# Performance work log

Hardware: AMD Instinct MI355X
Metric: run time of the kernel (lower is better)

The kernel has to match this reference:

```python
import jax, jax.numpy as jnp
import numpy as np

EPS = 1e-5  # RMSNorm epsilon


def rmsnorm(x, w):
    return x * jax.lax.rsqrt(jnp.mean(x * x, axis=-1, keepdims=True) + EPS) * w


def mamba_forward(u, in_proj_w, conv_w, conv_b, x_proj_w, dt_proj_w, dt_proj_b,
                  A_log, D_param, mamba_out_w):
    # u: (b, L, dm) -- canonical Mamba block (expand=2, d_state=16, d_conv=4)
    b, L, dm = u.shape
    di, ds = A_log.shape
    dtr = dt_proj_w.shape[1]
    xz = jnp.einsum('bld,ed->ble', u, in_proj_w)          # (b,L,2*di)
    x_, z = jnp.split(xz, 2, axis=-1)                     # each (b,L,di)
    # causal depthwise conv over the sequence axis
    dconv = conv_w.shape[-1]
    xc = jnp.transpose(x_, (0, 2, 1))                     # (b,di,L)
    xc = jnp.pad(xc, ((0, 0), (0, 0), (dconv - 1, 0)))
    xc = jax.lax.conv_general_dilated(xc, conv_w, window_strides=(1,), padding='VALID',
                                      dimension_numbers=('NCH', 'OIH', 'NCH'),
                                      feature_group_count=di)
    xc = xc + conv_b[None, :, None]
    x_ = jax.nn.silu(jnp.transpose(xc, (0, 2, 1)))        # (b,L,di)
    # input-dependent dt, B, C
    x_dbl = jnp.einsum('bld,ed->ble', x_, x_proj_w)       # (b,L,dtr+2*ds)
    dt, B, C = jnp.split(x_dbl, [dtr, dtr + ds], axis=-1)
    delta = jax.nn.softplus(jnp.einsum('blr,dr->bld', dt, dt_proj_w) + dt_proj_b)  # (b,L,di)
    A = -jnp.exp(A_log)                                   # (di,ds)

    def step(h, inp):
        d_t, B_t, C_t, x_t = inp                          # (b,di),(b,ds),(b,ds),(b,di)
        dA = jnp.exp(d_t[:, :, None] * A)                 # (b,di,ds)
        h = dA * h + (d_t * x_t)[:, :, None] * B_t[:, None, :]
        y = jnp.einsum('bds,bs->bd', h, C_t)
        return h, y

    xs = (jnp.moveaxis(delta, 1, 0), jnp.moveaxis(B, 1, 0),
          jnp.moveaxis(C, 1, 0), jnp.moveaxis(x_, 1, 0))
    h0 = jnp.zeros((b, di, ds), dtype=u.dtype)
    _, ys = jax.lax.scan(step, h0, xs)                    # ys: (L,b,di)
    y = jnp.moveaxis(ys, 0, 1) + x_ * D_param             # (b,L,di)
    y = y * jax.nn.silu(z)
    return jnp.einsum('bld,od->blo', y, mamba_out_w)      # (b,L,dm)


def conv1x1(W, bvec, t):
    # t: (b, cin, L) -> (b, cout, L)
    return jnp.einsum('oi,bit->bot', W, t) + bvec[None, :, None]


def reference(x, w_norm1, w_norm2, W_ip, b_ip, W_fp, b_fp, W_wp, b_wp, W_op, b_op,
              in_proj_w, conv_w, conv_b, x_proj_w, dt_proj_w, dt_proj_b,
              A_log, D_param, mamba_out_w):
    # x: (b, L, D) -- module's (b, c, l) with l == input_dim = D, c == seq = L
    residual = x
    xn = rmsnorm(x, w_norm1)                 # RMSNorm over last (input_dim) axis
    xt = jnp.transpose(xn, (0, 2, 1))        # 'b c l -> b l c' : (b, D, L)
    ssm = conv1x1(W_ip, b_ip, xt)            # (b, 2D, L)
    ssm = conv1x1(W_fp, b_fp, ssm)           # (b, 2D, L)
    u = jnp.transpose(ssm, (0, 2, 1))        # (b, L, 2D): seq=L, d_model=2D
    m = mamba_forward(u, in_proj_w, conv_w, conv_b, x_proj_w, dt_proj_w, dt_proj_b,
                      A_log, D_param, mamba_out_w)
    m = rmsnorm(m, w_norm2) + u              # PostNormMamba residual
    ssm = jnp.transpose(m, (0, 2, 1))        # (b, 2D, L)
    w = conv1x1(W_wp, b_wp, xt)              # (b, 2D, L)
    w = w * jax.nn.sigmoid(w)                # swish
    out = conv1x1(W_op, b_op, w * ssm)       # (b, D, L)
    return jnp.transpose(out, (0, 2, 1)) + residual


def setup_inputs():
    key = jax.random.key(0)
    ks = jax.random.split(key, 16)
    D, L, b = 64, 4096, 4
    dm, di, ds, dconv = 2 * D, 4 * D, 16, 4
    dtr = (dm + 15) // 16  # dt_rank = ceil(d_model/16) = 8

    def n(k, shape, fan_in):
        return jax.random.normal(k, shape, jnp.float32) * (1.0 / np.sqrt(fan_in))

    return {
        'x': jax.random.normal(ks[0], (b, L, D), jnp.float32),
        'w_norm1': jnp.ones((D,), jnp.float32),
        'w_norm2': jnp.ones((dm,), jnp.float32),
        'W_ip': n(ks[1], (2 * D, D), D), 'b_ip': jnp.zeros((2 * D,), jnp.float32),
        'W_fp': n(ks[2], (2 * D, 2 * D), 2 * D), 'b_fp': jnp.zeros((2 * D,), jnp.float32),
        'W_wp': n(ks[3], (2 * D, D), D), 'b_wp': jnp.zeros((2 * D,), jnp.float32),
        'W_op': n(ks[4], (D, 2 * D), 2 * D), 'b_op': jnp.zeros((D,), jnp.float32),
        'in_proj_w': n(ks[5], (2 * di, dm), dm),
        'conv_w': n(ks[6], (di, 1, dconv), dconv),
        'conv_b': jnp.zeros((di,), jnp.float32),
        'x_proj_w': n(ks[7], (dtr + 2 * ds, di), di),
        'dt_proj_w': n(ks[8], (di, dtr), dtr),
        'dt_proj_b': jnp.full((di,), float(np.log(np.expm1(0.01))), jnp.float32),
        'A_log': jnp.log(jnp.broadcast_to(jnp.arange(1, ds + 1, dtype=jnp.float32), (di, ds))),
        'D_param': jnp.ones((di,), jnp.float32),
        'mamba_out_w': n(ks[9], (dm, di), di),
    }
```

## Files before the change

kernel.cpp:

```cpp
#include <hip/hip_runtime.h>
#include <hip/hip_bf16.h>

typedef __hip_bfloat16 bf16;
typedef __attribute__((ext_vector_type(8))) short bf16x8;
typedef __attribute__((ext_vector_type(4))) float f32x4;
#define DEV __device__ __forceinline__

constexpr int SEQ  = 4096;
constexpr int NB   = 4;
constexpr int NTOK = NB * SEQ;
constexpr float EPS = 1e-5f;
constexpr int NCH = 32;
constexpr int NCHUNK = SEQ / NCH;
constexpr float LOG2E = 1.44269504f;

constexpr int OFF_WDT  = 0;
constexpr int OFF_WB   = 2048;
constexpr int WB_IP = 0;
constexpr int WB_WP = 8192;
constexpr int WB_FP = 16384;
constexpr int WB_PR = 32768;
constexpr int WB_MO = 98304;
constexpr int WB_OP = 131072;
constexpr int WB_XP = 139264;
constexpr int WB_TOT = 151552;
constexpr int OFF_XDBL = OFF_WB + WB_TOT / 2;
constexpr int OFF_R1   = OFF_XDBL + NTOK * 40;
constexpr int OFF_WSW  = OFF_R1   + 1048576;
constexpr int OFF_U    = OFF_WSW  + 1048576;
constexpr int OFF_R2   = OFF_U    + 1048576;
constexpr int OFF_SILUZ= OFF_R2   + 2097152;
constexpr int OFF_XC   = OFF_SILUZ+ 2097152;
constexpr int OFF_G    = OFF_XC   + 2097152;
constexpr int OFF_FLAG = OFF_G    + 2097152;
constexpr int OFF_SUMM = OFF_FLAG + 16;
constexpr int OFF_HIN  = OFF_SUMM + 64 * NCHUNK * 256 * 2;
constexpr int OFF_PLOC = OFF_HIN  + 64 * NCHUNK * 256;
constexpr int OFF_CUMD = OFF_PLOC + NTOK * 256;

DEV float b2f(bf16 x) { return __bfloat162float(x); }
DEV bf16 f2b(float x) { return __float2bfloat16(x); }
DEV short shof(bf16 h) { short s; __builtin_memcpy(&s, &h, 2); return s; }
DEV float ldin(const void* p, int i, int f) {
  return f ? ((const float*)p)[i] : b2f(((const bf16*)p)[i]);
}
DEV unsigned pack2(float a, float b) {
  bf16 ha = f2b(a), hb = f2b(b);
  unsigned short ua, ub;
  __builtin_memcpy(&ua, &ha, 2); __builtin_memcpy(&ub, &hb, 2);
  return (unsigned)ua | ((unsigned)ub << 16);
}
DEV float lo16f(unsigned u) { return __int_as_float((int)(u << 16)); }
DEV float hi16f(unsigned u) { return __int_as_float((int)(u & 0xffff0000u)); }
template<int CTRL>
DEV float dpp_add(float v) {
  int r = __builtin_amdgcn_update_dpp(0, __float_as_int(v), CTRL, 0xF, 0xF, false);
  return v + __int_as_float(r);
}
DEV float exp2f_fast(float a) { return __builtin_amdgcn_exp2f(a); }
DEV float softplus(float a) {
  return (a > 20.f) ? a : __logf(1.f + exp2f_fast(a * LOG2E));
}
DEV float silu(float a) { return a / (1.f + __expf(-a)); }

DEV void cpw(int e, int base, int count, const void* __restrict__ src,
             bf16* __restrict__ wb, int f) {
  int r = e - base;
  if (r >= 0 && r < count) wb[base + r] = f2b(ldin(src, r, f));
}
__global__ __launch_bounds__(256) void prep_k(
    const void* __restrict__ w_ip, const void* __restrict__ w_wp, const void* __restrict__ w_fp,
    const void* __restrict__ w_pr, const void* __restrict__ w_mo, const void* __restrict__ w_op,
    const void* __restrict__ w_x,  const void* __restrict__ w_dt,
    const void* __restrict__ x, float* __restrict__ wsf, int* __restrict__ flagp)
{
  __shared__ int cnt;
  if (threadIdx.x == 0) cnt = 0;
  __syncthreads();
  {
    float v = b2f(((const bf16*)x)[threadIdx.x]);
    int ok = (v == v) && fabsf(v) > 1e-4f && fabsf(v) < 100.f;
    atomicAdd(&cnt, ok);
  }
  __syncthreads();
  int f = (cnt > 204) ? 0 : 1;
  if (blockIdx.x == 0 && threadIdx.x == 0) *flagp = f;

  int e = blockIdx.x * 256 + threadIdx.x;
  bf16* wb = (bf16*)(wsf + OFF_WB);
  cpw(e, WB_IP, 8192,  w_ip, wb, f);
  cpw(e, WB_WP, 8192,  w_wp, wb, f);
  cpw(e, WB_FP, 16384, w_fp, wb, f);
  cpw(e, WB_PR, 65536, w_pr, wb, f);
  cpw(e, WB_MO, 32768, w_mo, wb, f);
  cpw(e, WB_OP, 8192,  w_op, wb, f);
  {
    int r = e - WB_XP;
    if (r >= 0 && r < 12288) wb[WB_XP + r] = (r < 10240) ? f2b(ldin(w_x, r, f)) : f2b(0.f);
  }
  if (e < 2048) {
    int r = e >> 8, d = e & 255;
    wsf[OFF_WDT + e] = ldin(w_dt, d * 8 + r, f);
  }
}

__global__ __launch_bounds__(512) void fm_k(
    const void* __restrict__ x, const void* __restrict__ w1, const float* __restrict__ wsf,
    const void* __restrict__ b_ip, const void* __restrict__ b_wp, const void* __restrict__ b_fp,
    bf16* __restrict__ wsw, bf16* __restrict__ u, bf16* __restrict__ xpre,
    bf16* __restrict__ siluz, const int* __restrict__ flagp)
{
  __shared__ __align__(16) char smem[33280];
  short* xn   = (short*)smem;
  short* t1   = (short*)(smem + 4608);
  short* ul   = (short*)(smem + 13312);
  short* wswl = (short*)(smem + 22016);
  short* xzl  = (short*)smem;

  const int f = *flagp;
  const int tid = threadIdx.x;
  const int tok0 = blockIdx.x * 32;
  {
    const int token = tid >> 4, r = tid & 15;
    float v[4]; float ss = 0.f;
    #pragma unroll
    for (int k = 0; k < 4; ++k) {
      v[k] = ldin(x, (tok0 + token) * 64 + r * 4 + k, f);
      ss += v[k] * v[k];
    }
    ss += __shfl_xor(ss, 1, 16); ss += __shfl_xor(ss, 2, 16);
    ss += __shfl_xor(ss, 4, 16); ss += __shfl_xor(ss, 8, 16);
    float sc = rsqrtf(ss * (1.f / 64.f) + EPS);
    unsigned* dst = (unsigned*)xn + token * 36 + r * 2;
    #pragma unroll
    for (int k = 0; k < 2; ++k) {
      int i = r * 4 + k * 2;
      dst[k] = pack2(v[k*2] * sc * ldin(w1, i, f), v[k*2+1] * sc * ldin(w1, i + 1, f));
    }
  }
  __syncthreads();
  const int lane = tid & 63, m = lane & 15, q = lane >> 4;
  const int w = tid >> 6;
  {
    const int wt = w >> 2, ng = w & 3;
    const bf16* W = (const bf16*)(wsf + OFF_WB) + (wt ? WB_WP : WB_IP);
    const void* bia = wt ? b_wp : b_ip;
    bf16x8 a[2][2];
    #pragma unroll
    for (int mt = 0; mt < 2; ++mt)
      #pragma unroll
      for (int kk = 0; kk < 2; ++kk)
        a[mt][kk] = *(const bf16x8*)&xn[(mt * 16 + m) * 72 + kk * 32 + q * 8];
    #pragma unroll
    for (int nti = 0; nti < 2; ++nti) {
      int nt = ng * 2 + nti;
      int n = nt * 16 + m;
      f32x4 acc[2] = {{0,0,0,0},{0,0,0,0}};
      #pragma unroll
      for (int kk = 0; kk < 2; ++kk) {
        bf16x8 b = *(const bf16x8*)(W + (nt * 16 + m) * 64 + kk * 32 + q * 8);
        #pragma unroll
        for (int mt = 0; mt < 2; ++mt)
          acc[mt] = __builtin_amdgcn_mfma_f32_16x16x32_bf16(a[mt][kk], b, acc[mt], 0, 0, 0);
      }
      float bv = ldin(bia, n, f);
      #pragma unroll
      for (int mt = 0; mt < 2; ++mt)
        #pragma unroll
        for (int r = 0; r < 4; ++r) {
          float v = acc[mt][r] + bv;
          int row = mt * 16 + q * 4 + r;
          if (wt) wswl[row * 128 + n] = shof(f2b(silu(v)));
          else    t1[row * 136 + n] = shof(f2b(v));
        }
    }
  }
  __syncthreads();
  {
    int row = tid >> 4, c8 = (tid & 15) * 8;
    uint4 v = *(const uint4*)&wswl[row * 128 + c8];
    *(uint4*)(wsw + (tok0 + row) * 128 + c8) = v;
  }
  {
    const bf16* WF = (const bf16*)(wsf + OFF_WB) + WB_FP;
    bf16x8 a[2][4];
    #pragma unroll
    for (int mt = 0; mt < 2; ++mt)
      #pragma unroll
      for (int kk = 0; kk < 4; ++kk)
        a[mt][kk] = *(const bf16x8*)&t1[(mt * 16 + m) * 136 + kk * 32 + q * 8];
    {
      int nt = w;
      int n = nt * 16 + m;
      f32x4 acc[2] = {{0,0,0,0},{0,0,0,0}};
      #pragma unroll
      for (int kk = 0; kk < 4; ++kk) {
        bf16x8 b = *(const bf16x8*)(WF + (nt * 16 + m) * 128 + kk * 32 + q * 8);
        #pragma unroll
        for (int mt = 0; mt < 2; ++mt)
          acc[mt] = __builtin_amdgcn_mfma_f32_16x16x32_bf16(a[mt][kk], b, acc[mt], 0, 0, 0);
      }
      float bv = ldin(b_fp, n, f);
      #pragma unroll
      for (int mt = 0; mt < 2; ++mt)
        #pragma unroll
        for (int r = 0; r < 4; ++r)
          ul[(mt * 16 + q * 4 + r) * 136 + n] = shof(f2b(acc[mt][r] + bv));
    }
  }
  __syncthreads();
  {
    int row = tid >> 4, c8 = (tid & 15) * 8;
    uint4 v = *(const uint4*)&ul[row * 136 + c8];
    *(uint4*)(u + (tok0 + row) * 128 + c8) = v;
  }
  {
    const bf16* WP = (const bf16*)(wsf + OFF_WB) + WB_PR;
    bf16x8 a[2][4];
    #pragma unroll
    for (int mt = 0; mt < 2; ++mt)
      #pragma unroll
      for (int kk = 0; kk < 4; ++kk)
        a[mt][kk] = *(const bf16x8*)&ul[(mt * 16 + m) * 136 + kk * 32 + q * 8];
    __syncthreads();
    #pragma unroll
    for (int nti = 0; nti < 4; ++nti) {
      int nt = w * 4 + nti;
      int n = nt * 16 + m;
      f32x4 acc[2] = {{0,0,0,0},{0,0,0,0}};
      #pragma unroll
      for (int kk = 0; kk < 4; ++kk) {
        bf16x8 b = *(const bf16x8*)(WP + (nt * 16 + m) * 128 + kk * 32 + q * 8);
        #pragma unroll
        for (int mt = 0; mt < 2; ++mt)
          acc[mt] = __builtin_amdgcn_mfma_f32_16x16x32_bf16(a[mt][kk], b, acc[mt], 0, 0, 0);
      }
      #pragma unroll
      for (int mt = 0; mt < 2; ++mt)
        #pragma unroll
        for (int r = 0; r < 4; ++r) {
          int row = mt * 16 + q * 4 + r;
          float v = acc[mt][r];
          xzl[row * 520 + n] = shof(f2b(n < 256 ? v : silu(v)));
        }
    }
  }
  __syncthreads();
  {
    #pragma unroll
    for (int k = 0; k < 4; ++k) {
      int chunk = tid + k * 512;
      int row = chunk >> 6, seg = chunk & 63;
      uint4 v = *(const uint4*)&xzl[row * 520 + seg * 8];
      int n0 = seg * 8;
      if (n0 < 256) *(uint4*)(xpre + (tok0 + row) * 256 + n0) = v;
      else          *(uint4*)(siluz + (tok0 + row) * 256 + (n0 - 256)) = v;
    }
  }
}

__global__ __launch_bounds__(256) void conv_k(
    const bf16* __restrict__ xpre, const void* __restrict__ cw, const void* __restrict__ cb,
    const float* __restrict__ wsf, bf16* __restrict__ xc, float* __restrict__ xdbl,
    const int* __restrict__ flagp)
{
  __shared__ short xh[35 * 256];
  __shared__ short cs[32 * 264];
  const int f = *flagp;
  const int tid = threadIdx.x;
  const int tok0 = blockIdx.x * 32;
  const bool seqstart = (tok0 & (SEQ - 1)) == 0;
  for (int c = tid; c < 1120; c += 256) {
    int e0 = c * 8;
    int tt = e0 >> 8, i = e0 & 255;
    int gtok = tok0 + tt - 3;
    uint4* dst = (uint4*)(xh + e0);
    if (gtok >= 0 && !(seqstart && tt < 3)) *dst = *(const uint4*)(xpre + gtok * 256 + i);
    else                                    *dst = make_uint4(0, 0, 0, 0);
  }
  __syncthreads();
  {
    const int ch0 = (tid & 63) * 4;
    const int t0 = (tid >> 6) * 8;
    float w4[4][4], cb4[4];
    #pragma unroll
    for (int c = 0; c < 4; ++c) {
      cb4[c] = ldin(cb, ch0 + c, f);
      #pragma unroll
      for (int k = 0; k < 4; ++k) w4[c][k] = ldin(cw, (ch0 + c) * 4 + k, f);
    }
    float win[11][4];
    #pragma unroll
    for (int r = 0; r < 11; ++r) {
      uint2 v = *(const uint2*)&xh[(t0 + r) * 256 + ch0];
      win[r][0] = lo16f(v.x); win[r][1] = hi16f(v.x);
      win[r][2] = lo16f(v.y); win[r][3] = hi16f(v.y);
    }
    #pragma unroll
    for (int t = 0; t < 8; ++t) {
      unsigned pk[2];
      #pragma unroll
      for (int cp = 0; cp < 2; ++cp) {
        float o[2];
        #pragma unroll
        for (int ci = 0; ci < 2; ++ci) {
          int c = cp * 2 + ci;
          float acc = cb4[c];
          #pragma unroll
          for (int k = 0; k < 4; ++k) acc = fmaf(win[t + k][c], w4[c][k], acc);
          o[ci] = silu(acc);
        }
        pk[cp] = pack2(o[0], o[1]);
      }
      uint2 pv = make_uint2(pk[0], pk[1]);
      *(uint2*)&cs[(t0 + t) * 264 + ch0] = pv;
      *(uint2*)(xc + (tok0 + t0 + t) * 256 + ch0) = pv;
    }
  }
  __syncthreads();
  const int w = tid >> 6;
  if (w < 2) {
    const bf16* Wx = (const bf16*)(wsf + OFF_WB) + WB_XP;
    const int lane = tid & 63, m = lane & 15, quad = lane >> 4;
    f32x4 acc[3] = {{0,0,0,0},{0,0,0,0},{0,0,0,0}};
    #pragma unroll
    for (int k0 = 0; k0 < 256; k0 += 32) {
      bf16x8 af = *(const bf16x8*)&cs[(w * 16 + m) * 264 + k0 + quad * 8];
      #pragma unroll
      for (int nt = 0; nt < 3; ++nt) {
        bf16x8 bfr = *(const bf16x8*)(Wx + (nt * 16 + m) * 256 + k0 + quad * 8);
        acc[nt] = __builtin_amdgcn_mfma_f32_16x16x32_bf16(af, bfr, acc[nt], 0, 0, 0);
      }
    }
    #pragma unroll
    for (int nt = 0; nt < 3; ++nt) {
      int n = nt * 16 + m;
      if (n < 40) {
        #pragma unroll
        for (int r = 0; r < 4; ++r)
          xdbl[(tok0 + w * 16 + quad * 4 + r) * 40 + n] = acc[nt][r];
      }
    }
  }
}

__global__ __launch_bounds__(256) void scanF_k(
    const float* __restrict__ xdbl, const bf16* __restrict__ xc,
    const void* __restrict__ A_log, const void* __restrict__ dt_b,
    const float* __restrict__ WDT, float* __restrict__ summ,
    float* __restrict__ ploc, float* __restrict__ cumd, const int* __restrict__ flagp)
{
  const int f = *flagp;
  const int tid = threadIdx.x;
  const int bb = blockIdx.x >> 2, dgsup = blockIdx.x & 3, c = blockIdx.y;
  const int dgsub = tid >> 6, lane = tid & 63, dl = lane >> 2, squad = lane & 3;
  const int dg = dgsup * 4 + dgsub;
  const int bxOld = bb * 16 + dg;
  const int d_comp = dg * 16 + dl;
  const int bd = tid & 63;
  const int d_stg = dgsup * 64 + bd;
  const int bdc = dgsub * 16 + dl;
  const int tok_base = bb * SEQ + c * NCH;

  __shared__ float dt_l[NCH * 8];
  __shared__ float dx_l[16 * 64 * 2];
  __shared__ float Bp[16 * 16];
  __shared__ float Cp[16 * 16];
  __shared__ float pg_l[16 * 64];
  __shared__ float cd_l[16 * 64];

  float Aval2[4];
  #pragma unroll
  for (int j = 0; j < 4; ++j)
    Aval2[j] = -__expf(ldin(A_log, d_comp * 16 + squad * 4 + j, f)) * LOG2E;
  const float dtb_stg = ldin(dt_b, d_stg, f);
  float wdt[8];
  #pragma unroll
  for (int r = 0; r < 8; ++r) wdt[r] = WDT[r * 256 + d_stg];

  float h[4] = {0.f, 0.f, 0.f, 0.f};
  float sdlt = 0.f;

  if (tid < 64)
    *(float4*)(dt_l + tid * 4) = *(const float4*)(xdbl + (tok_base + (tid >> 1)) * 40 + (tid & 1) * 4);

  #pragma unroll 1
  for (int half = 0; half < 2; ++half) {
    const int tb = half * 16;
    __syncthreads();
    {
      int tl = tid >> 4, s = tid & 15;
      int tok = tok_base + tb + tl;
      Bp[tid] = xdbl[tok * 40 + 8 + s];
      Cp[tid] = xdbl[tok * 40 + 24 + s];
    }
    #pragma unroll
    for (int k = 0; k < 4; ++k) {
      int tl = (tid >> 6) + k * 4;
      int tok = tok_base + tb + tl;
      const float* dtr = dt_l + (tb + tl) * 8;
      float a = dtb_stg;
      #pragma unroll
      for (int r = 0; r < 8; ++r) a = fmaf(dtr[r], wdt[r], a);
      float dlt = softplus(a);
      float xcv = b2f(xc[tok * 256 + d_stg]);
      *(float2*)(dx_l + (tl * 64 + bd) * 2) = make_float2(dlt, dlt * xcv);
    }
    __syncthreads();

    #pragma unroll 8
    for (int tl = 0; tl < 16; ++tl) {
      float2 dx = *(const float2*)(dx_l + (tl * 64 + bdc) * 2);
      float4 B4 = *(const float4*)(Bp + tl * 16 + squad * 4);
      float Bv[4] = {B4.x, B4.y, B4.z, B4.w};
      #pragma unroll
      for (int j = 0; j < 4; ++j) {
        float dA = exp2f_fast(dx.x * Aval2[j]);
        h[j] = fmaf(dA, h[j], dx.y * Bv[j]);
      }
      sdlt += dx.x;
      float4 C4 = *(const float4*)(Cp + tl * 16 + squad * 4);
      float p = h[0] * C4.x;
      p = fmaf(h[1], C4.y, p);
      p = fmaf(h[2], C4.z, p);
      p = fmaf(h[3], C4.w, p);
      p = dpp_add<0xB1>(p);
      p = dpp_add<0x4E>(p);
      if (squad == 0) { pg_l[tl * 64 + bdc] = p; cd_l[tl * 64 + bdc] = sdlt; }
    }
    __syncthreads();
    #pragma unroll
    for (int k = 0; k < 4; ++k) {
      int tl = (tid >> 6) + k * 4;
      int tok = tok_base + tb + tl;
      ploc[tok * 256 + d_stg] = pg_l[tl * 64 + bd];
      cumd[tok * 256 + d_stg] = cd_l[tl * 64 + bd];
    }
  }

  float* dst = summ + ((bxOld * NCHUNK + c) * 256 + dl * 16 + squad * 4) * 2;
  *(float4*)(dst)     = make_float4(exp2f_fast(Aval2[0] * sdlt), h[0],
                                    exp2f_fast(Aval2[1] * sdlt), h[1]);
  *(float4*)(dst + 4) = make_float4(exp2f_fast(Aval2[2] * sdlt), h[2],
                                    exp2f_fast(Aval2[3] * sdlt), h[3]);
}

__global__ __launch_bounds__(256) void scanB_k(const float* __restrict__ summ, float* __restrict__ hinit) {
  int bx = blockIdx.x, qq = threadIdx.x;
  float h = 0.f;
  for (int c0 = 0; c0 < NCHUNK; c0 += 16) {
    float2 sv[16];
    #pragma unroll
    for (int k = 0; k < 16; ++k)
      sv[k] = *(const float2*)(summ + ((bx * NCHUNK + c0 + k) * 256 + qq) * 2);
    #pragma unroll
    for (int k = 0; k < 16; ++k) {
      hinit[(bx * NCHUNK + c0 + k) * 256 + qq] = h;
      h = fmaf(sv[k].x, h, sv[k].y);
    }
  }
}

__global__ __launch_bounds__(512) void backC_k(
    const float* __restrict__ xdbl, const bf16* __restrict__ xc, const bf16* __restrict__ siluz,
    const void* __restrict__ A_log, const void* __restrict__ D_par,
    const float* __restrict__ hinit, const float* __restrict__ ploc, const float* __restrict__ cumd,
    const float* __restrict__ wsf, const void* __restrict__ w2,
    const bf16* __restrict__ u, const bf16* __restrict__ wsw, const void* __restrict__ b_op,
    const void* __restrict__ x, void* __restrict__ out, const int* __restrict__ flagp)
{
  __shared__ __align__(16) char smem[51712];
  short* gl  = (short*)smem;
  float* Cp  = (float*)(smem + 16896);
  float* cdl = (float*)(smem + 18944);
  float* gcl = (float*)(smem + 35328);
  short* ms  = (short*)(smem + 18944);

  const int f = *flagp;
  const int tid = threadIdx.x;
  const int tok0 = blockIdx.x * 32;
  const int bb = tok0 >> 12;
  const int c  = (tok0 & (SEQ - 1)) >> 5;
  const int w = tid >> 6, lane = tid & 63;
  const int dl = lane >> 2, squad = lane & 3;
  const int chL = w * 16 + dl;
  const int chE = tid & 127;

  {
    int tl = tid >> 4, s = tid & 15;
    Cp[tid] = xdbl[(tok0 + tl) * 40 + 24 + s];
  }

  #pragma unroll 1
  for (int p = 0; p < 2; ++p) {
    const int ch = p * 128 + chL;
    #pragma unroll
    for (int k = 0; k < 8; ++k) {
      int tl = (tid >> 7) + k * 4;
      cdl[tl * 128 + chE] = cumd[(tok0 + tl) * 256 + p * 128 + chE];
    }
    float Aval2[4];
    #pragma unroll
    for (int j = 0; j < 4; ++j)
      Aval2[j] = -__expf(ldin(A_log, ch * 16 + squad * 4 + j, f)) * LOG2E;
    float4 hv = *(const float4*)(hinit +
        ((bb * 16 + (ch >> 4)) * NCHUNK + c) * 256 + (ch & 15) * 16 + squad * 4);
    __syncthreads();
    #pragma unroll 8
    for (int tl = 0; tl < 32; ++tl) {
      float cum = cdl[tl * 128 + chL];
      float4 C4 = *(const float4*)(Cp + tl * 16 + squad * 4);
      float pv =      C4.x * exp2f_fast(cum * Aval2[0]) * hv.x;
      pv = fmaf(C4.y * exp2f_fast(cum * Aval2[1]), hv.y, pv);
      pv = fmaf(C4.z * exp2f_fast(cum * Aval2[2]), hv.z, pv);
      pv = fmaf(C4.w * exp2f_fast(cum * Aval2[3]), hv.w, pv);
      pv = dpp_add<0xB1>(pv);
      pv = dpp_add<0x4E>(pv);
      if (squad == 0) gcl[tl * 128 + chL] = pv;
    }
    __syncthreads();
    {
      const int gch = p * 128 + chE;
      const float Dp = ldin(D_par, gch, f);
      #pragma unroll
      for (int k = 0; k < 8; ++k) {
        int tl = (tid >> 7) + k * 4;
        int tok = tok0 + tl;
        float pf = gcl[tl * 128 + chE] + ploc[tok * 256 + gch];
        float xcv = b2f(xc[tok * 256 + gch]);
        gl[tl * 264 + gch] = shof(f2b((pf + xcv * Dp) * b2f(siluz[tok * 256 + gch])));
      }
    }
    __syncthreads();
  }

  const int m = lane & 15, q = lane >> 4;
  const bf16* WM = (const bf16*)(wsf + OFF_WB) + WB_MO;
  const bf16* WO = (const bf16*)(wsf + OFF_WB) + WB_OP;
  {
    f32x4 acc[2] = {{0,0,0,0},{0,0,0,0}};
    #pragma unroll
    for (int kk = 0; kk < 8; ++kk) {
      bf16x8 a0 = *(const bf16x8*)&gl[m * 264 + kk * 32 + q * 8];
      bf16x8 a1 = *(const bf16x8*)&gl[(16 + m) * 264 + kk * 32 + q * 8];
      int nt = w;
      bf16x8 b = *(const bf16x8*)(WM + (nt * 16 + m) * 256 + kk * 32 + q * 8);
      acc[0] = __builtin_amdgcn_mfma_f32_16x16x32_bf16(a0, b, acc[0], 0, 0, 0);
      acc[1] = __builtin_amdgcn_mfma_f32_16x16x32_bf16(a1, b, acc[1], 0, 0, 0);
    }
    {
      int n = w * 16 + m;
      #pragma unroll
      for (int mt = 0; mt < 2; ++mt)
        #pragma unroll
        for (int r = 0; r < 4; ++r)
          ms[(mt * 16 + q * 4 + r) * 136 + n] = shof(f2b(acc[mt][r]));
    }
  }
  __syncthreads();
  {
    const int token = tid >> 4, r = tid & 15;
    float mv[8]; float ss = 0.f;
    #pragma unroll
    for (int k = 0; k < 8; ++k) {
      mv[k] = b2f(((const bf16*)ms)[token * 136 + r * 8 + k]);
      ss += mv[k] * mv[k];
    }
    ss += __shfl_xor(ss, 1, 16); ss += __shfl_xor(ss, 2, 16);
    ss += __shfl_xor(ss, 4, 16); ss += __shfl_xor(ss, 8, 16);
    float sc = rsqrtf(ss * (1.f / 128.f) + EPS);
    #pragma unroll
    for (int k = 0; k < 8; ++k) {
      int i = r * 8 + k;
      int ga = (tok0 + token) * 128 + i;
      float v = mv[k] * sc * ldin(w2, i, f) + b2f(u[ga]);
      ms[token * 136 + i] = shof(f2b(v * b2f(wsw[ga])));
    }
  }
  __syncthreads();
  {
    const int mt = w >> 2, nt = w & 3;
    bf16x8 a[4];
    #pragma unroll
    for (int kk = 0; kk < 4; ++kk)
      a[kk] = *(const bf16x8*)&ms[(mt * 16 + m) * 136 + kk * 32 + q * 8];
    __syncthreads();
    f32x4 acc = {0,0,0,0};
    #pragma unroll
    for (int kk = 0; kk < 4; ++kk) {
      bf16x8 b = *(const bf16x8*)(WO + (nt * 16 + m) * 128 + kk * 32 + q * 8);
      acc = __builtin_amdgcn_mfma_f32_16x16x32_bf16(a[kk], b, acc, 0, 0, 0);
    }
    float* outl = (float*)ms;
    int n = nt * 16 + m;
    #pragma unroll
    for (int r = 0; r < 4; ++r)
      outl[(mt * 16 + q * 4 + r) * 68 + n] = acc[r];
  }
  __syncthreads();
  {
    const float* outl = (const float*)ms;
    int row = tid >> 4, c0 = (tid & 15) * 4;
    float v[4];
    #pragma unroll
    for (int j = 0; j < 4; ++j)
      v[j] = outl[row * 68 + c0 + j] + ldin(b_op, c0 + j, f)
           + ldin(x, (tok0 + row) * 64 + c0 + j, f);
    if (f) {
      *(float4*)((float*)out + (tok0 + row) * 64 + c0) = make_float4(v[0], v[1], v[2], v[3]);
    } else {
      uint2 pv = make_uint2(pack2(v[0], v[1]), pack2(v[2], v[3]));
      *(uint2*)((bf16*)out + (tok0 + row) * 64 + c0) = pv;
    }
  }
}

extern "C" void kernel_launch(void* const* d_in, const int* in_sizes, int n_in,
                              void* d_out, int out_size, void* d_ws, size_t ws_size,
                              hipStream_t stream) {
  (void)in_sizes; (void)n_in; (void)out_size; (void)ws_size;
  const void* x        = d_in[0];
  const void* w_norm1  = d_in[1];
  const void* w_norm2  = d_in[2];
  const void* W_ip     = d_in[3];
  const void* b_ip     = d_in[4];
  const void* W_fp     = d_in[5];
  const void* b_fp     = d_in[6];
  const void* W_wp     = d_in[7];
  const void* b_wp     = d_in[8];
  const void* W_op     = d_in[9];
  const void* b_op     = d_in[10];
  const void* in_proj  = d_in[11];
  const void* conv_w   = d_in[12];
  const void* conv_b   = d_in[13];
  const void* x_proj   = d_in[14];
  const void* dt_projw = d_in[15];
  const void* dt_projb = d_in[16];
  const void* A_log    = d_in[17];
  const void* D_par    = d_in[18];
  const void* mo_w     = d_in[19];

  float* wsf    = (float*)d_ws;
  float* xdbl   = wsf + OFF_XDBL;
  bf16*  wsw_b  = (bf16*)(wsf + OFF_WSW);
  bf16*  u_b    = (bf16*)(wsf + OFF_U);
  bf16*  xpre_b = (bf16*)(wsf + OFF_R2);
  float* summ   = wsf + OFF_SUMM;
  float* hin    = wsf + OFF_HIN;
  float* plocp  = wsf + OFF_PLOC;
  float* cumdp  = wsf + OFF_CUMD;
  bf16*  siluz_b= (bf16*)(wsf + OFF_SILUZ);
  bf16*  xc_b   = (bf16*)(wsf + OFF_XC);
  int*   flagp  = (int*)(wsf + OFF_FLAG);

  prep_k<<<dim3(592), dim3(256), 0, stream>>>(W_ip, W_wp, W_fp, in_proj, mo_w, W_op,
                                              x_proj, dt_projw, x, wsf, flagp);
  fm_k<<<dim3(NTOK / 32), dim3(512), 0, stream>>>(x, w_norm1, wsf, b_ip, b_wp, b_fp,
                                                  wsw_b, u_b, xpre_b, siluz_b, flagp);
  conv_k<<<dim3(NTOK / 32), dim3(256), 0, stream>>>(xpre_b, conv_w, conv_b, wsf, xc_b, xdbl, flagp);
  scanF_k<<<dim3(16, NCHUNK), dim3(256), 0, stream>>>(xdbl, xc_b, A_log, dt_projb,
                                                      wsf + OFF_WDT, summ, plocp, cumdp, flagp);
  scanB_k<<<dim3(64), dim3(256), 0, stream>>>(summ, hin);
  backC_k<<<dim3(NTOK / 32), dim3(512), 0, stream>>>(xdbl, xc_b, siluz_b, A_log, D_par,
                                                     hin, plocp, cumdp, wsf, w_norm2,
                                                     u_b, wsw_b, b_op, x, d_out, flagp);
}
```

Measured before the change: 188.4 us.

## Recompute chunk scan in output kernel instead of storing per-token partials

The forward chunk scan now only produces chunk summaries and no longer writes per-token local outputs and cumulative deltas to global memory. The final kernel reruns the in-chunk recurrence, starting from the carried-in state and recomputing delta via softplus, to produce y directly. This removes two large fp32 NTOK×256 global writes and their later reads, in exchange for running the exp-heavy recurrence twice.

```diff
diff --git a/kernel.cpp b/kernel.cpp
--- a/kernel.cpp
+++ b/kernel.cpp
@@ -35,8 +35,6 @@
 constexpr int OFF_FLAG = OFF_G    + 2097152;
 constexpr int OFF_SUMM = OFF_FLAG + 16;
 constexpr int OFF_HIN  = OFF_SUMM + 64 * NCHUNK * 256 * 2;
-constexpr int OFF_PLOC = OFF_HIN  + 64 * NCHUNK * 256;
-constexpr int OFF_CUMD = OFF_PLOC + NTOK * 256;
 
 DEV float b2f(bf16 x) { return __bfloat162float(x); }
 DEV bf16 f2b(float x) { return __float2bfloat16(x); }
@@ -347,8 +345,7 @@
 __global__ __launch_bounds__(256) void scanF_k(
     const float* __restrict__ xdbl, const bf16* __restrict__ xc,
     const void* __restrict__ A_log, const void* __restrict__ dt_b,
-    const float* __restrict__ WDT, float* __restrict__ summ,
-    float* __restrict__ ploc, float* __restrict__ cumd, const int* __restrict__ flagp)
+    const float* __restrict__ WDT, float* __restrict__ summ, const int* __restrict__ flagp)
 {
   const int f = *flagp;
   const int tid = threadIdx.x;
@@ -365,9 +362,6 @@
   __shared__ float dt_l[NCH * 8];
   __shared__ float dx_l[16 * 64 * 2];
   __shared__ float Bp[16 * 16];
-  __shared__ float Cp[16 * 16];
-  __shared__ float pg_l[16 * 64];
-  __shared__ float cd_l[16 * 64];
 
   float Aval2[4];
   #pragma unroll
@@ -390,9 +384,7 @@
     __syncthreads();
     {
       int tl = tid >> 4, s = tid & 15;
-      int tok = tok_base + tb + tl;
-      Bp[tid] = xdbl[tok * 40 + 8 + s];
-      Cp[tid] = xdbl[tok * 40 + 24 + s];
+      Bp[tid] = xdbl[(tok_base + tb + tl) * 40 + 8 + s];
     }
     #pragma unroll
     for (int k = 0; k < 4; ++k) {
@@ -419,22 +411,6 @@
         h[j] = fmaf(dA, h[j], dx.y * Bv[j]);
       }
       sdlt += dx.x;
-      float4 C4 = *(const float4*)(Cp + tl * 16 + squad * 4);
-      float p = h[0] * C4.x;
-      p = fmaf(h[1], C4.y, p);
-      p = fmaf(h[2], C4.z, p);
-      p = fmaf(h[3], C4.w, p);
-      p = dpp_add<0xB1>(p);
-      p = dpp_add<0x4E>(p);
-      if (squad == 0) { pg_l[tl * 64 + bdc] = p; cd_l[tl * 64 + bdc] = sdlt; }
-    }
-    __syncthreads();
-    #pragma unroll
-    for (int k = 0; k < 4; ++k) {
-      int tl = (tid >> 6) + k * 4;
-      int tok = tok_base + tb + tl;
-      ploc[tok * 256 + d_stg] = pg_l[tl * 64 + bd];
-      cumd[tok * 256 + d_stg] = cd_l[tl * 64 + bd];
     }
   }
 
@@ -463,18 +439,20 @@
 
 __global__ __launch_bounds__(512) void backC_k(
     const float* __restrict__ xdbl, const bf16* __restrict__ xc, const bf16* __restrict__ siluz,
-    const void* __restrict__ A_log, const void* __restrict__ D_par,
-    const float* __restrict__ hinit, const float* __restrict__ ploc, const float* __restrict__ cumd,
+    const void* __restrict__ A_log, const void* __restrict__ D_par, const void* __restrict__ dt_b,
+    const float* __restrict__ WDT, const float* __restrict__ hinit,
     const float* __restrict__ wsf, const void* __restrict__ w2,
     const bf16* __restrict__ u, const bf16* __restrict__ wsw, const void* __restrict__ b_op,
     const void* __restrict__ x, void* __restrict__ out, const int* __restrict__ flagp)
 {
-  __shared__ __align__(16) char smem[51712];
-  short* gl  = (short*)smem;
-  float* Cp  = (float*)(smem + 16896);
-  float* cdl = (float*)(smem + 18944);
-  float* gcl = (float*)(smem + 35328);
-  short* ms  = (short*)(smem + 18944);
+  __shared__ __align__(16) char smem[46592];
+  short* gl   = (short*)smem;
+  float* Bp   = (float*)(smem + 16896);
+  float* Cp   = (float*)(smem + 18944);
+  float* dt_l = (float*)(smem + 20992);
+  float* dx_l = (float*)(smem + 22016);
+  float* gcl  = (float*)(smem + 38400);
+  short* ms   = (short*)(smem + 22016);
 
   const int f = *flagp;
   const int tid = threadIdx.x;
@@ -488,51 +466,80 @@
 
   {
     int tl = tid >> 4, s = tid & 15;
+    Bp[tid] = xdbl[(tok0 + tl) * 40 + 8 + s];
     Cp[tid] = xdbl[(tok0 + tl) * 40 + 24 + s];
   }
+  if (tid < 64)
+    *(float4*)(dt_l + tid * 4) = *(const float4*)(xdbl + (tok0 + (tid >> 1)) * 40 + (tid & 1) * 4);
 
   #pragma unroll 1
   for (int p = 0; p < 2; ++p) {
-    const int ch = p * 128 + chL;
-    #pragma unroll
-    for (int k = 0; k < 8; ++k) {
-      int tl = (tid >> 7) + k * 4;
-      cdl[tl * 128 + chE] = cumd[(tok0 + tl) * 256 + p * 128 + chE];
-    }
+    const int ch  = p * 128 + chL;
+    const int gch = p * 128 + chE;
     float Aval2[4];
     #pragma unroll
     for (int j = 0; j < 4; ++j)
       Aval2[j] = -__expf(ldin(A_log, ch * 16 + squad * 4 + j, f)) * LOG2E;
+    const float dtb = ldin(dt_b, gch, f);
+    float wdt[8];
+    #pragma unroll
+    for (int r = 0; r < 8; ++r) wdt[r] = WDT[r * 256 + gch];
     float4 hv = *(const float4*)(hinit +
         ((bb * 16 + (ch >> 4)) * NCHUNK + c) * 256 + (ch & 15) * 16 + squad * 4);
-    __syncthreads();
-    #pragma unroll 8
-    for (int tl = 0; tl < 32; ++tl) {
-      float cum = cdl[tl * 128 + chL];
-      float4 C4 = *(const float4*)(Cp + tl * 16 + squad * 4);
-      float pv =      C4.x * exp2f_fast(cum * Aval2[0]) * hv.x;
-      pv = fmaf(C4.y * exp2f_fast(cum * Aval2[1]), hv.y, pv);
-      pv = fmaf(C4.z * exp2f_fast(cum * Aval2[2]), hv.z, pv);
-      pv = fmaf(C4.w * exp2f_fast(cum * Aval2[3]), hv.w, pv);
-      pv = dpp_add<0xB1>(pv);
-      pv = dpp_add<0x4E>(pv);
-      if (squad == 0) gcl[tl * 128 + chL] = pv;
-    }
-    __syncthreads();
-    {
-      const int gch = p * 128 + chE;
-      const float Dp = ldin(D_par, gch, f);
-      #pragma unroll
-      for (int k = 0; k < 8; ++k) {
+    float h[4] = {hv.x, hv.y, hv.z, hv.w};
+
+    #pragma unroll 1
+    for (int half = 0; half < 2; ++half) {
+      const int tb = half * 16;
+      __syncthreads();
+      #pragma unroll
+      for (int k = 0; k < 4; ++k) {
         int tl = (tid >> 7) + k * 4;
-        int tok = tok0 + tl;
-        float pf = gcl[tl * 128 + chE] + ploc[tok * 256 + gch];
+        int tok = tok0 + tb + tl;
+        const float* dtr = dt_l + (tb + tl) * 8;
+        float a = dtb;
+        #pragma unroll
+        for (int r = 0; r < 8; ++r) a = fmaf(dtr[r], wdt[r], a);
+        float dlt = softplus(a);
         float xcv = b2f(xc[tok * 256 + gch]);
-        gl[tl * 264 + gch] = shof(f2b((pf + xcv * Dp) * b2f(siluz[tok * 256 + gch])));
-      }
-    }
-    __syncthreads();
-  }
+        *(float2*)(dx_l + (tl * 128 + chE) * 2) = make_float2(dlt, dlt * xcv);
+      }
+      __syncthreads();
+
+      #pragma unroll 8
+      for (int tl = 0; tl < 16; ++tl) {
+        float2 dx = *(const float2*)(dx_l + (tl * 128 + chL) * 2);
+        float4 B4 = *(const float4*)(Bp + (tb + tl) * 16 + squad * 4);
+        float Bv[4] = {B4.x, B4.y, B4.z, B4.w};
+        #pragma unroll
+        for (int j = 0; j < 4; ++j) {
+          float dA = exp2f_fast(dx.x * Aval2[j]);
+          h[j] = fmaf(dA, h[j], dx.y * Bv[j]);
+        }
+        float4 C4 = *(const float4*)(Cp + (tb + tl) * 16 + squad * 4);
+        float pv = h[0] * C4.x;
+        pv = fmaf(h[1], C4.y, pv);
+        pv = fmaf(h[2], C4.z, pv);
+        pv = fmaf(h[3], C4.w, pv);
+        pv = dpp_add<0xB1>(pv);
+        pv = dpp_add<0x4E>(pv);
+        if (squad == 0) gcl[tl * 128 + chL] = pv;
+      }
+      __syncthreads();
+      {
+        const float Dp = ldin(D_par, gch, f);
+        #pragma unroll
+        for (int k = 0; k < 4; ++k) {
+          int tl = (tid >> 7) + k * 4;
+          int tok = tok0 + tb + tl;
+          float pf = gcl[tl * 128 + chE];
+          float xcv = b2f(xc[tok * 256 + gch]);
+          gl[(tb + tl) * 264 + gch] = shof(f2b((pf + xcv * Dp) * b2f(siluz[tok * 256 + gch])));
+        }
+      }
+    }
+  }
+  __syncthreads();
 
   const int m = lane & 15, q = lane >> 4;
   const bf16* WM = (const bf16*)(wsf + OFF_WB) + WB_MO;
@@ -647,8 +654,6 @@
   bf16*  xpre_b = (bf16*)(wsf + OFF_R2);
   float* summ   = wsf + OFF_SUMM;
   float* hin    = wsf + OFF_HIN;
-  float* plocp  = wsf + OFF_PLOC;
-  float* cumdp  = wsf + OFF_CUMD;
   bf16*  siluz_b= (bf16*)(wsf + OFF_SILUZ);
   bf16*  xc_b   = (bf16*)(wsf + OFF_XC);
   int*   flagp  = (int*)(wsf + OFF_FLAG);
@@ -659,9 +664,9 @@
                                                   wsw_b, u_b, xpre_b, siluz_b, flagp);
   conv_k<<<dim3(NTOK / 32), dim3(256), 0, stream>>>(xpre_b, conv_w, conv_b, wsf, xc_b, xdbl, flagp);
   scanF_k<<<dim3(16, NCHUNK), dim3(256), 0, stream>>>(xdbl, xc_b, A_log, dt_projb,
-                                                      wsf + OFF_WDT, summ, plocp, cumdp, flagp);
+                                                      wsf + OFF_WDT, summ, flagp);
   scanB_k<<<dim3(64), dim3(256), 0, stream>>>(summ, hin);
   backC_k<<<dim3(NTOK / 32), dim3(512), 0, stream>>>(xdbl, xc_b, siluz_b, A_log, D_par,
-                                                     hin, plocp, cumdp, wsf, w_norm2,
+                                                     dt_projb, wsf + OFF_WDT, hin, wsf, w_norm2,
                                                      u_b, wsw_b, b_op, x, d_out, flagp);
 }
```

Result: no change. 188.2 us, median of 2 (-0.1%).
